# Kernel optimization log

Hardware: AMD Instinct MI355X
Metric: run time of the kernel (lower is better)

The kernel has to match this reference:

```python
import jax, jax.numpy as jnp
import numpy as np

B, S, D, H = 2, 2048, 1024, 16
DH = D // H  # key_dim = embed_dim // num_heads
NEG = 1e9    # Keras masked-softmax adder magnitude
EPS = 1e-6


def setup_inputs() -> dict:
    key = jax.random.key(0)
    ks = jax.random.split(key, 6)
    sc = 1.0 / np.sqrt(D)
    return {
        "x": jax.random.normal(ks[0], (B, S, D), jnp.float32),
        "Wq": jax.random.normal(ks[1], (D, H, DH), jnp.float32) * sc,
        "bq": jnp.zeros((H, DH), jnp.float32),
        "Wk": jax.random.normal(ks[2], (D, H, DH), jnp.float32) * sc,
        "bk": jnp.zeros((H, DH), jnp.float32),
        "Wv": jax.random.normal(ks[3], (D, H, DH), jnp.float32) * sc,
        "bv": jnp.zeros((H, DH), jnp.float32),
        "Wo": jax.random.normal(ks[4], (H, DH, D), jnp.float32) * (1.0 / np.sqrt(D)),
        "bo": jnp.zeros((D,), jnp.float32),
        "gamma": jnp.ones((D,), jnp.float32),
        "beta": jnp.zeros((D,), jnp.float32),
    }


def reference(x, Wq, bq, Wk, bk, Wv, bv, Wo, bo, gamma, beta):
    # Keras MultiHeadAttention(query=x, value=x), inference (dropouts are identity)
    q = jnp.einsum("bsd,dhk->bshk", x, Wq) + bq  # [B,S,H,DH]
    k = jnp.einsum("bsd,dhk->bshk", x, Wk) + bk
    v = jnp.einsum("bsd,dhk->bshk", x, Wv) + bv

    scores = jnp.einsum("bqhd,bkhd->bhqk", q, k) / jnp.sqrt(jnp.asarray(DH, x.dtype))
    # Source: mask = 1 - band_part(ones, -1, 0) -> ones strictly ABOVE diagonal.
    # Keras attends where mask==1 and adds (1-mask)*(-1e9) elsewhere. Faithful:
    i = jnp.arange(S)[:, None]
    j = jnp.arange(S)[None, :]
    allowed = (j > i).astype(scores.dtype)  # [S,S], strict upper triangle
    scores = scores + (allowed - 1.0) * NEG  # subtract 1e9 where not allowed
    probs = jax.nn.softmax(scores, axis=-1)

    ctx = jnp.einsum("bhqk,bkhd->bqhd", probs, v)  # [B,S,H,DH]
    attn_out = jnp.einsum("bqhd,hdo->bqo", ctx, Wo) + bo  # [B,S,D]

    # residual + LayerNorm(eps=1e-6)
    y = x + attn_out
    mu = jnp.mean(y, axis=-1, keepdims=True)
    var = jnp.mean(jnp.square(y - mu), axis=-1, keepdims=True)
    return (y - mu) * jax.lax.rsqrt(var + EPS) * gamma + beta
```

## Files before the change

### kernel.cpp

```cpp
#include <hip/hip_runtime.h>
#include <hip/hip_bf16.h>

typedef __hip_bfloat16 bf16;
typedef __attribute__((ext_vector_type(8))) short bf16x8;
typedef __attribute__((ext_vector_type(4))) float f32x4;

constexpr int Bc  = 2;
constexpr int Sc  = 2048;
constexpr int Dc  = 1024;
constexpr int Hc  = 16;
constexpr int DHc = 64;
constexpr int BS  = Bc * Sc;
constexpr int NT  = Sc / 64;

__device__ __forceinline__ float bs2f(unsigned short u) {
    union { unsigned int i; float f; } v; v.i = ((unsigned int)u) << 16; return v.f;
}
__device__ __forceinline__ short f2bs(float x) {
    bf16 h = __float2bfloat16(x);
    return *reinterpret_cast<short*>(&h);
}

typedef const __attribute__((address_space(1))) unsigned int* as1_u32p;
typedef __attribute__((address_space(3))) unsigned int* as3_u32p;
__device__ __forceinline__ void gl_lds16(const void* g, void* l) {
    __builtin_amdgcn_global_load_lds((as1_u32p)g, (as3_u32p)l, 16, 0, 0);
}

__global__ __launch_bounds__(256) void cast_x(const float* __restrict__ in,
                                              short* __restrict__ out) {
    const int i = (blockIdx.x * 256 + threadIdx.x) * 4;
    const float4 v = *(const float4*)(in + i);
    ushort4 o;
    o.x = (unsigned short)f2bs(v.x);
    o.y = (unsigned short)f2bs(v.y);
    o.z = (unsigned short)f2bs(v.z);
    o.w = (unsigned short)f2bs(v.w);
    *(ushort4*)(out + i) = o;
}

__global__ __launch_bounds__(256) void transpose_cast(
    const float* __restrict__ w0, const float* __restrict__ w1,
    const float* __restrict__ w2, const float* __restrict__ w3,
    short* __restrict__ outbase)
{
    __shared__ float T[64][65];
    const int z = blockIdx.z;
    const float* in = (z == 0) ? w0 : (z == 1) ? w1 : (z == 2) ? w2 : w3;
    short* out = outbase + (size_t)z * 1024 * 1024;
    const int k0 = blockIdx.x * 64, n0 = blockIdx.y * 64;
    const int t = threadIdx.x;
    #pragma unroll
    for (int it = 0; it < 4; ++it) {
        const int s = it * 256 + t;
        const int r = s >> 4, c = (s & 15) * 4;
        *(float4*)&T[r][c] = *(const float4*)(in + (size_t)(k0 + r) * 1024 + n0 + c);
    }
    __syncthreads();
    #pragma unroll
    for (int it = 0; it < 4; ++it) {
        const int s = it * 256 + t;
        const int rr = s >> 4, cc = (s & 15) * 4;
        ushort4 o;
        o.x = (unsigned short)f2bs(T[cc + 0][rr]);
        o.y = (unsigned short)f2bs(T[cc + 1][rr]);
        o.z = (unsigned short)f2bs(T[cc + 2][rr]);
        o.w = (unsigned short)f2bs(T[cc + 3][rr]);
        *(ushort4*)(out + (size_t)(n0 + rr) * 1024 + k0 + cc) = o;
    }
}

__global__ __launch_bounds__(256, 3) void gemm_bt(
    const short* __restrict__ A, const short* __restrict__ BTbase,
    const float* __restrict__ b0, const float* __restrict__ b1,
    const float* __restrict__ b2, short* __restrict__ Cbase)
{
    __shared__ __align__(16) short As[128 * 64];
    __shared__ __align__(16) short Bs[128 * 64];

    const int z = blockIdx.z;
    const short* BT = BTbase + (size_t)z * 1024 * 1024;
    const float* bias = (z == 0) ? b0 : (z == 1) ? b1 : b2;
    short* C = Cbase + (size_t)z * BS * Dc;

    const int t = threadIdx.x;
    const int lane = t & 63, w = t >> 6;
    const int quad = lane >> 4, l16 = lane & 15;
    const int wm = (w & 1) * 64, wn = (w >> 1) * 64;
    const int row0 = blockIdx.y * 128;
    const int col0 = blockIdx.x * 128;
    const int sw = l16 & 7;

    f32x4 acc[4][4] = {};

    for (int kt = 0; kt < 1024; kt += 64) {
        __syncthreads();
        #pragma unroll
        for (int i = 0; i < 4; ++i) {
            const int f = i * 256 + t;
            const int r = f >> 3;
            const int g = (f & 7) ^ (r & 7);
            short* lb = &As[(i * 256 + w * 64) * 8];
            gl_lds16(A + (size_t)(row0 + r) * 1024 + kt + g * 8, lb);
            short* lb2 = &Bs[(i * 256 + w * 64) * 8];
            gl_lds16(BT + (size_t)(col0 + r) * 1024 + kt + g * 8, lb2);
        }
        __syncthreads();
        #pragma unroll
        for (int ks = 0; ks < 2; ++ks) {
            bf16x8 av[4], bv[4];
            #pragma unroll
            for (int mt = 0; mt < 4; ++mt) {
                const int r = wm + mt * 16 + l16;
                av[mt] = *(const bf16x8*)&As[r * 64 + ((ks * 4 + quad) ^ sw) * 8];
            }
            #pragma unroll
            for (int nt = 0; nt < 4; ++nt) {
                const int r = wn + nt * 16 + l16;
                bv[nt] = *(const bf16x8*)&Bs[r * 64 + ((ks * 4 + quad) ^ sw) * 8];
            }
            #pragma unroll
            for (int mt = 0; mt < 4; ++mt)
                #pragma unroll
                for (int nt = 0; nt < 4; ++nt)
                    acc[mt][nt] = __builtin_amdgcn_mfma_f32_16x16x32_bf16(
                        av[mt], bv[nt], acc[mt][nt], 0, 0, 0);
        }
    }

    float bvv[4];
    #pragma unroll
    for (int nt = 0; nt < 4; ++nt) bvv[nt] = bias[col0 + wn + nt * 16 + l16];
    #pragma unroll
    for (int mt = 0; mt < 4; ++mt)
        #pragma unroll
        for (int reg = 0; reg < 4; ++reg) {
            const size_t row = row0 + wm + mt * 16 + quad * 4 + reg;
            #pragma unroll
            for (int nt = 0; nt < 4; ++nt) {
                const int col = col0 + wn + nt * 16 + l16;
                C[row * 1024 + col] = f2bs(acc[mt][nt][reg] + bvv[nt]);
            }
        }
}

__device__ __forceinline__ void qtile_step(
    const bf16x8 (&qf)[2], const bf16x8 (&kf)[2][4],
    const short (&VsT)[64][72], short (&Psw)[16][72],
    const int k0, const int row_base,
    const int quad, const int l16,
    float (&l)[4], f32x4 (&O)[4])
{
    f32x4 S[4] = {};
    #pragma unroll
    for (int ks = 0; ks < 2; ++ks)
        #pragma unroll
        for (int nt = 0; nt < 4; ++nt)
            S[nt] = __builtin_amdgcn_mfma_f32_16x16x32_bf16(qf[ks], kf[ks][nt], S[nt], 0, 0, 0);

    #pragma unroll
    for (int nt = 0; nt < 4; ++nt) {
        const int col = k0 + nt * 16 + l16;
        #pragma unroll
        for (int reg = 0; reg < 4; ++reg) {
            const int row = row_base + quad * 4 + reg;
            const float s = (col > row) ? fminf(S[nt][reg] * 0.125f, 80.f) : -87.0f;
            const float p = __expf(s);
            S[nt][reg] = p;
            l[reg] += p;
        }
    }

    #pragma unroll
    for (int nt = 0; nt < 4; ++nt)
        #pragma unroll
        for (int reg = 0; reg < 4; ++reg)
            Psw[quad * 4 + reg][nt * 16 + l16] = f2bs(S[nt][reg]);

    #pragma unroll
    for (int ks = 0; ks < 2; ++ks) {
        const bf16x8 pf = *(const bf16x8*)&Psw[l16][ks * 32 + quad * 8];
        #pragma unroll
        for (int nt = 0; nt < 4; ++nt) {
            const bf16x8 vf = *(const bf16x8*)&VsT[nt * 16 + l16][ks * 32 + quad * 8];
            O[nt] = __builtin_amdgcn_mfma_f32_16x16x32_bf16(pf, vf, O[nt], 0, 0, 0);
        }
    }
}

__global__ __launch_bounds__(512, 4) void attn_mfma(
    const short* __restrict__ Qg, const short* __restrict__ Kg,
    const short* __restrict__ Vg, short* __restrict__ CTX)
{
    __shared__ __align__(16) short Ks [64][72];
    __shared__ __align__(16) short VsT[64][72];
    __shared__ __align__(16) short Ps[8][16][72];

    const int tid  = threadIdx.x;
    const int lane = tid & 63, w = tid >> 6;
    const int quad = lane >> 4, l16 = lane & 15;
    const int wq   = w & 3;
    const bool isA = (w < 4);
    const int p  = blockIdx.x;
    const int h  = blockIdx.y;
    const int b  = blockIdx.z;
    const size_t rb = (size_t)b * Sc;
    const int cb = h * DHc;

    const int myT0 = isA ? p : (NT - 1 - p);
    const int q0   = myT0 * 64;

    bf16x8 qf[2];
    {
        const short* qp = Qg + (rb + q0 + wq * 16 + l16) * (size_t)Dc + cb + quad * 8;
        qf[0] = *(const bf16x8*)(qp);
        qf[1] = *(const bf16x8*)(qp + 32);
    }

    float l[4] = {};
    f32x4 O[4] = {};

    const int skey = tid & 63, sseg = (tid >> 6) * 8;

    {
        const size_t g = (rb + p * 64 + skey) * (size_t)Dc + cb + sseg;
        const bf16x8 kv = *(const bf16x8*)(Kg + g);
        const bf16x8 vv = *(const bf16x8*)(Vg + g);
        *(bf16x8*)&Ks[skey][sseg] = kv;
        #pragma unroll
        for (int e = 0; e < 8; ++e) VsT[sseg + e][skey] = vv[e];
    }
    __syncthreads();

    for (int t = p; t < NT; ++t) {
        const bool havenext = (t + 1 < NT);
        bf16x8 pk, pv;
        if (havenext) {
            const size_t g = (rb + (t + 1) * 64 + skey) * (size_t)Dc + cb + sseg;
            pk = *(const bf16x8*)(Kg + g);
            pv = *(const bf16x8*)(Vg + g);
        }

        if (t >= myT0) {
            bf16x8 kf[2][4];
            #pragma unroll
            for (int ks = 0; ks < 2; ++ks)
                #pragma unroll
                for (int nt = 0; nt < 4; ++nt)
                    kf[ks][nt] = *(const bf16x8*)&Ks[nt * 16 + l16][ks * 32 + quad * 8];
            qtile_step(qf, kf, VsT, Ps[w], t * 64, q0 + wq * 16, quad, l16, l, O);
        }

        if (havenext) {
            __syncthreads();
            *(bf16x8*)&Ks[skey][sseg] = pk;
            #pragma unroll
            for (int e = 0; e < 8; ++e) VsT[sseg + e][skey] = pv[e];
            __syncthreads();
        }
    }

    #pragma unroll
    for (int off = 1; off < 16; off <<= 1)
        #pragma unroll
        for (int reg = 0; reg < 4; ++reg)
            l[reg] += __shfl_xor(l[reg], off, 64);
    #pragma unroll
    for (int reg = 0; reg < 4; ++reg) l[reg] = 1.0f / l[reg];
    #pragma unroll
    for (int nt = 0; nt < 4; ++nt)
        #pragma unroll
        for (int reg = 0; reg < 4; ++reg) {
            const size_t row = rb + q0 + wq * 16 + quad * 4 + reg;
            CTX[row * Dc + cb + nt * 16 + l16] = f2bs(O[nt][reg] * l[reg]);
        }
}

__global__ __launch_bounds__(256) void vmean(const short* __restrict__ V,
                                             short* __restrict__ CTX)
{
    const int h = blockIdx.x, b = blockIdx.y;
    const int t = threadIdx.x;
    const int dh = t & 63, ck = t >> 6;
    float s = 0.f;
    const short* vp = V + ((size_t)b * Sc + ck * 512) * Dc + h * DHc + dh;
    for (int j = 0; j < 512; ++j) s += bs2f(vp[(size_t)j * Dc]);
    __shared__ float red[4][64];
    red[ck][dh] = s;
    __syncthreads();
    if (ck == 0) {
        const float tot = (red[0][dh] + red[1][dh] + red[2][dh] + red[3][dh]) * (1.f / Sc);
        CTX[((size_t)b * Sc + Sc - 1) * Dc + h * DHc + dh] = f2bs(tot);
    }
}

__global__ __launch_bounds__(256, 4) void resid_ln(
    const float* __restrict__ X, const short* __restrict__ AO,
    const float* __restrict__ gamma, const float* __restrict__ beta,
    float* __restrict__ out)
{
    const int r = blockIdx.x;
    const int t = threadIdx.x;
    const size_t base = (size_t)r * Dc + t * 4;

    const float4 x4 = *(const float4*)(X + base);
    const ushort4 a4 = *(const ushort4*)(AO + base);
    float y[4];
    y[0] = x4.x + bs2f(a4.x);
    y[1] = x4.y + bs2f(a4.y);
    y[2] = x4.z + bs2f(a4.z);
    y[3] = x4.w + bs2f(a4.w);

    float s  = y[0] + y[1] + y[2] + y[3];
    float s2 = y[0]*y[0] + y[1]*y[1] + y[2]*y[2] + y[3]*y[3];
    #pragma unroll
    for (int off = 1; off < 64; off <<= 1) {
        s  += __shfl_xor(s,  off, 64);
        s2 += __shfl_xor(s2, off, 64);
    }
    __shared__ float red[8];
    const int w = t >> 6;
    if ((t & 63) == 0) { red[w] = s; red[4 + w] = s2; }
    __syncthreads();
    s  = red[0] + red[1] + red[2] + red[3];
    s2 = red[4] + red[5] + red[6] + red[7];

    const float mu   = s * (1.0f / Dc);
    const float rstd = rsqrtf(s2 * (1.0f / Dc) - mu * mu + 1e-6f);

    const float4 g4 = *(const float4*)(gamma + t * 4);
    const float4 b4 = *(const float4*)(beta  + t * 4);
    float4 o;
    o.x = (y[0] - mu) * rstd * g4.x + b4.x;
    o.y = (y[1] - mu) * rstd * g4.y + b4.y;
    o.z = (y[2] - mu) * rstd * g4.z + b4.z;
    o.w = (y[3] - mu) * rstd * g4.w + b4.w;
    *(float4*)(out + base) = o;
}

extern "C" void kernel_launch(void* const* d_in, const int* in_sizes, int n_in,
                              void* d_out, int out_size, void* d_ws, size_t ws_size,
                              hipStream_t stream)
{
    (void)in_sizes; (void)n_in; (void)out_size; (void)ws_size;
    const float* x     = (const float*)d_in[0];
    const float* Wq    = (const float*)d_in[1];
    const float* bq    = (const float*)d_in[2];
    const float* Wk    = (const float*)d_in[3];
    const float* bk    = (const float*)d_in[4];
    const float* Wv    = (const float*)d_in[5];
    const float* bv    = (const float*)d_in[6];
    const float* Wo    = (const float*)d_in[7];
    const float* bo    = (const float*)d_in[8];
    const float* gamma = (const float*)d_in[9];
    const float* beta  = (const float*)d_in[10];
    float* out = (float*)d_out;

    const size_t matN = (size_t)BS * Dc;
    const size_t wN   = (size_t)Dc * Dc;
    short* xb = (short*)d_ws;
    short* WT = xb + matN;
    short* Qb = WT + 4 * wN;
    short* Kb = Qb + matN;
    short* Vb = Kb + matN;
    short* Cx = Vb + matN;
    short* AO = Qb;

    cast_x<<<matN / 1024, 256, 0, stream>>>(x, xb);

    dim3 gt(16, 16, 4);
    transpose_cast<<<gt, 256, 0, stream>>>(Wq, Wk, Wv, Wo, WT);

    dim3 gq(Dc / 128, BS / 128, 3);
    gemm_bt<<<gq, 256, 0, stream>>>(xb, WT, bq, bk, bv, Qb);

    dim3 ga(16, Hc, Bc);
    attn_mfma<<<ga, 512, 0, stream>>>(Qb, Kb, Vb, Cx);

    dim3 gv(Hc, Bc);
    vmean<<<gv, 256, 0, stream>>>(Vb, Cx);

    dim3 go(Dc / 128, BS / 128, 1);
    gemm_bt<<<go, 256, 0, stream>>>(Cx, WT + 3 * wN, bo, bo, bo, AO);

    resid_ln<<<BS, 256, 0, stream>>>(x, AO, gamma, beta, out);
}
```

Measured before the change: 226.6 us.

## Double-buffer K/V tiles in LDS, specialize diagonal mask, pad P scratch

K and V shared-memory tiles are now double-buffered so the next tile can be stored while the current one is consumed, which removes one of the two block barriers per iteration. The causal mask comparison is applied only on the diagonal tile through a template parameter, so off-diagonal tiles skip the index math. The per-warp P scratch gets an extra padding offset every four rows to reduce LDS bank conflicts. The cost is twice the LDS for K/V, which could lower occupancy at 512 threads per block.

```diff
diff --git a/kernel.cpp b/kernel.cpp
--- a/kernel.cpp
+++ b/kernel.cpp
@@ -144,13 +144,26 @@
         }
 }
 
+__device__ __forceinline__ int psw_off(int row, int col) {
+    return row * 72 + (row >> 2) * 48 + col;
+}
+
+template<bool DIAG>
 __device__ __forceinline__ void qtile_step(
-    const bf16x8 (&qf)[2], const bf16x8 (&kf)[2][4],
-    const short (&VsT)[64][72], short (&Psw)[16][72],
+    const bf16x8 (&qf)[2],
+    const short (&Ks)[64][72], const short (&VsT)[64][72],
+    short* __restrict__ Psw,
     const int k0, const int row_base,
     const int quad, const int l16,
     float (&l)[4], f32x4 (&O)[4])
 {
+    bf16x8 kf[2][4];
+    #pragma unroll
+    for (int ks = 0; ks < 2; ++ks)
+        #pragma unroll
+        for (int nt = 0; nt < 4; ++nt)
+            kf[ks][nt] = *(const bf16x8*)&Ks[nt * 16 + l16][ks * 32 + quad * 8];
+
     f32x4 S[4] = {};
     #pragma unroll
     for (int ks = 0; ks < 2; ++ks)
@@ -160,11 +173,14 @@
 
     #pragma unroll
     for (int nt = 0; nt < 4; ++nt) {
-        const int col = k0 + nt * 16 + l16;
         #pragma unroll
         for (int reg = 0; reg < 4; ++reg) {
-            const int row = row_base + quad * 4 + reg;
-            const float s = (col > row) ? fminf(S[nt][reg] * 0.125f, 80.f) : -87.0f;
+            float s = fminf(S[nt][reg] * 0.125f, 80.f);
+            if (DIAG) {
+                const int col = k0 + nt * 16 + l16;
+                const int row = row_base + quad * 4 + reg;
+                s = (col > row) ? s : -87.0f;
+            }
             const float p = __expf(s);
             S[nt][reg] = p;
             l[reg] += p;
@@ -175,11 +191,11 @@
     for (int nt = 0; nt < 4; ++nt)
         #pragma unroll
         for (int reg = 0; reg < 4; ++reg)
-            Psw[quad * 4 + reg][nt * 16 + l16] = f2bs(S[nt][reg]);
+            Psw[psw_off(quad * 4 + reg, nt * 16 + l16)] = f2bs(S[nt][reg]);
 
     #pragma unroll
     for (int ks = 0; ks < 2; ++ks) {
-        const bf16x8 pf = *(const bf16x8*)&Psw[l16][ks * 32 + quad * 8];
+        const bf16x8 pf = *(const bf16x8*)&Psw[psw_off(l16, ks * 32 + quad * 8)];
         #pragma unroll
         for (int nt = 0; nt < 4; ++nt) {
             const bf16x8 vf = *(const bf16x8*)&VsT[nt * 16 + l16][ks * 32 + quad * 8];
@@ -192,9 +208,9 @@
     const short* __restrict__ Qg, const short* __restrict__ Kg,
     const short* __restrict__ Vg, short* __restrict__ CTX)
 {
-    __shared__ __align__(16) short Ks [64][72];
-    __shared__ __align__(16) short VsT[64][72];
-    __shared__ __align__(16) short Ps[8][16][72];
+    __shared__ __align__(16) short Ks [2][64][72];
+    __shared__ __align__(16) short VsT[2][64][72];
+    __shared__ __align__(16) short Ps[8][1296];
 
     const int tid  = threadIdx.x;
     const int lane = tid & 63, w = tid >> 6;
@@ -223,16 +239,18 @@
     const int skey = tid & 63, sseg = (tid >> 6) * 8;
 
     {
+        const int buf = p & 1;
         const size_t g = (rb + p * 64 + skey) * (size_t)Dc + cb + sseg;
         const bf16x8 kv = *(const bf16x8*)(Kg + g);
         const bf16x8 vv = *(const bf16x8*)(Vg + g);
-        *(bf16x8*)&Ks[skey][sseg] = kv;
-        #pragma unroll
-        for (int e = 0; e < 8; ++e) VsT[sseg + e][skey] = vv[e];
+        *(bf16x8*)&Ks[buf][skey][sseg] = kv;
+        #pragma unroll
+        for (int e = 0; e < 8; ++e) VsT[buf][sseg + e][skey] = vv[e];
     }
     __syncthreads();
 
     for (int t = p; t < NT; ++t) {
+        const int cur = t & 1;
         const bool havenext = (t + 1 < NT);
         bf16x8 pk, pv;
         if (havenext) {
@@ -241,21 +259,18 @@
             pv = *(const bf16x8*)(Vg + g);
         }
 
-        if (t >= myT0) {
-            bf16x8 kf[2][4];
+        if (t > myT0) {
+            qtile_step<false>(qf, Ks[cur], VsT[cur], Ps[w],
+                              t * 64, q0 + wq * 16, quad, l16, l, O);
+        } else if (t == myT0) {
+            qtile_step<true>(qf, Ks[cur], VsT[cur], Ps[w],
+                             t * 64, q0 + wq * 16, quad, l16, l, O);
+        }
+
+        if (havenext) {
+            *(bf16x8*)&Ks[cur ^ 1][skey][sseg] = pk;
             #pragma unroll
-            for (int ks = 0; ks < 2; ++ks)
-                #pragma unroll
-                for (int nt = 0; nt < 4; ++nt)
-                    kf[ks][nt] = *(const bf16x8*)&Ks[nt * 16 + l16][ks * 32 + quad * 8];
-            qtile_step(qf, kf, VsT, Ps[w], t * 64, q0 + wq * 16, quad, l16, l, O);
-        }
-
-        if (havenext) {
-            __syncthreads();
-            *(bf16x8*)&Ks[skey][sseg] = pk;
-            #pragma unroll
-            for (int e = 0; e < 8; ++e) VsT[sseg + e][skey] = pv[e];
+            for (int e = 0; e < 8; ++e) VsT[cur ^ 1][sseg + e][skey] = pv[e];
             __syncthreads();
         }
     }
```

Measured after the change: 222.8 us. Within noise of the previous version (-1.7%).
